# Optimization experiments

Hardware: AMD Instinct MI355X
Metric: run time of the kernel (lower is better)

## Reference

```python
import jax, jax.numpy as jnp
import numpy as np
from functools import partial

EPS = 1e-5
PATCH = 3
STYLE_STRENGTH = 1.0


def _whiten_color_mats(x):
    # x: (b, c, n) already flattened; returns mean, eigvecs, eigvals of covariance
    mean = x.mean(axis=-1, keepdims=True)
    xc = x - mean
    n = x.shape[-1]
    cov = jnp.einsum('bcn,bdn->bcd', xc, xc) / (n - 1)
    evals, evecs = jnp.linalg.eigh(cov)
    evals = jnp.maximum(evals, EPS)
    return mean, xc, evecs, evals


def whitening(x):
    b, c, h, w = x.shape
    xf = x.reshape(b, c, h * w)
    _, xc, E, d = _whiten_color_mats(xf)
    # W = E diag(d^-1/2) E^T
    Wm = jnp.einsum('bce,be,bde->bcd', E, d ** -0.5, E)
    return jnp.einsum('bcd,bdn->bcn', Wm, xc).reshape(b, c, h, w)


def coloring(x, style):
    b, c, h, w = x.shape
    xf = x.reshape(b, c, h * w)
    sf = style.reshape(b, c, -1)
    smean, sc, E, d = _whiten_color_mats(sf)
    Cm = jnp.einsum('bce,be,bde->bcd', E, d ** 0.5, E)
    out = jnp.einsum('bcd,bdn->bcn', Cm, xf) + smean
    return out.reshape(b, c, h, w)


def extract_style_kernels(style):
    # returns (b, hw, c, 3, 3) patches and (b, hw, 1, 1, 1) L2 norms
    b, c, H, W = style.shape
    p = jnp.pad(style, ((0, 0), (0, 0), (1, 1), (1, 1)), mode='reflect')
    patches = jnp.stack([p[:, :, i:i + H, j:j + W]
                         for i in range(PATCH) for j in range(PATCH)], axis=-1)  # (b,c,H,W,9)
    k = patches.reshape(b, c, H * W, PATCH * PATCH).transpose(0, 2, 1, 3)  # (b,hw,c,9)
    norm = jnp.sqrt(jnp.sum(k * k, axis=(2, 3))) + EPS  # (b,hw)
    return k.reshape(b, H * W, c, PATCH, PATCH), norm[:, :, None, None, None]


_DN = ('NCHW', 'OIHW', 'NCHW')


def _conv_per_sample(feat, kern):
    # feat (c,H,W), kern (o,c,3,3): reflect-pad 1, VALID conv -> (o,H,W)
    fp = jnp.pad(feat, ((0, 0), (1, 1), (1, 1)), mode='reflect')
    out = jax.lax.conv_general_dilated(fp[None], kern, (1, 1), 'VALID',
                                       dimension_numbers=_DN)
    return out[0]


def _deconv_per_sample(onehot, kern):
    # conv_transpose2d(stride=1, padding=2) == VALID conv with flipped, transposed kernel
    kt = jnp.flip(kern, axis=(-2, -1)).transpose(1, 0, 2, 3)  # (c, hw, 3, 3)
    fp = jnp.pad(onehot, ((0, 0), (1, 1), (1, 1)), mode='reflect')
    out = jax.lax.conv_general_dilated(fp[None], kt, (1, 1), 'VALID',
                                       dimension_numbers=_DN)
    return out[0]


def norm_deconvolution(h, w, patch_size):
    full = np.zeros((h + patch_size - 1, w + patch_size - 1), dtype=np.float32)
    for x in range(patch_size):
        for y in range(patch_size):
            full[y:y + h, x:x + w] += 1.0
    pw = (patch_size - 1) // 2
    if pw > 0:
        full = full[pw:-pw, pw:-pw]
    return jnp.asarray(full)[None, None]  # (1,1,h,w)


def reassemble_feature(nc, ns):
    b, c, H, W = nc.shape
    hw = H * W
    kern, norm = extract_style_kernels(ns)
    score = jax.vmap(_conv_per_sample)(nc, kern / norm)  # (b, hw, H, W)
    idx = jnp.argmax(score, axis=1)  # (b, H, W)
    onehot = (jnp.arange(hw, dtype=idx.dtype)[None, :, None, None] == idx[:, None]
              ).astype(nc.dtype)  # (b, hw, H, W)
    recon = jax.vmap(_deconv_per_sample)(onehot, kern)  # (b, c, H, W)
    return recon / norm_deconvolution(H, W, PATCH).astype(recon.dtype)


def setup_inputs() -> dict:
    key = jax.random.key(0)
    k1, k2 = jax.random.split(key)
    content_feature = jax.random.normal(k1, (2, 256, 64, 64), dtype=jnp.float32)
    style_feature = jax.random.normal(k2, (2, 256, 64, 64), dtype=jnp.float32)
    return {"content_feature": content_feature, "style_feature": style_feature}


def reference(content_feature, style_feature):
    nc = whitening(content_feature)
    ns = whitening(style_feature)
    reassembled = reassemble_feature(nc, ns)
    stylized = coloring(reassembled, style_feature)
    return (1.0 - STYLE_STRENGTH) * content_feature + STYLE_STRENGTH * stylized
```

## Files before the change

kernel.cpp:

```cpp
#include <hip/hip_runtime.h>
#include <hip/hip_bf16.h>

#define C_ 256
#define N_ 4096
#define CN (C_*N_)
#define EPSF 1e-5f
#define NS_ITERS 6
#define KSPLIT 16
#define LSTR 40

typedef _Float16 f16x8 __attribute__((ext_vector_type(8)));
typedef float f32x4 __attribute__((ext_vector_type(4)));

__device__ __forceinline__ int refl(int t) {
  return t < 0 ? -t : (t > 63 ? 126 - t : t);
}

__device__ __forceinline__ unsigned short f2h(float x) {
  _Float16 h = (_Float16)x;
  return __builtin_bit_cast(unsigned short, h);
}
__device__ __forceinline__ float h2f(unsigned short u) {
  return (float)__builtin_bit_cast(_Float16, u);
}

__device__ __forceinline__ void mm64_3term(unsigned short* sm, const float* A, const float* B,
                                           int m0, int n0, f32x4 acc[2][2]) {
  const int P = 64*LSTR;
  int t = threadIdx.x;
  int lane = t & 63;
  int wv = (t >> 7) & 1, wu = (t >> 6) & 1;
  int lx16 = lane & 15, quad = lane >> 4;
  int srow = t >> 2, sseg = (t & 3) * 8;
#pragma unroll
  for (int i = 0; i < 2; i++)
#pragma unroll
    for (int j = 0; j < 2; j++) acc[i][j] = (f32x4){0.f, 0.f, 0.f, 0.f};
  for (int k0 = 0; k0 < 256; k0 += 32) {
    __syncthreads();
    {
      const float* pa = &A[(size_t)(m0 + srow)*256 + k0 + sseg];
      const float* pb = &B[(size_t)(n0 + srow)*256 + k0 + sseg];
#pragma unroll
      for (int g = 0; g < 2; g++) {
        float4 va = *(const float4*)(pa + g*4);
        float4 vb = *(const float4*)(pb + g*4);
        float fa[4] = {va.x, va.y, va.z, va.w};
        float fb[4] = {vb.x, vb.y, vb.z, vb.w};
        unsigned short ha[4], la[4], hb[4], lb[4];
#pragma unroll
        for (int j = 0; j < 4; j++) {
          unsigned short h = f2h(fa[j]); ha[j] = h; la[j] = f2h(fa[j] - h2f(h));
          h = f2h(fb[j]); hb[j] = h; lb[j] = f2h(fb[j] - h2f(h));
        }
        int lo_ = srow*LSTR + sseg + g*4;
        *(ushort4*)&sm[0*P + lo_] = make_ushort4(ha[0], ha[1], ha[2], ha[3]);
        *(ushort4*)&sm[1*P + lo_] = make_ushort4(la[0], la[1], la[2], la[3]);
        *(ushort4*)&sm[2*P + lo_] = make_ushort4(hb[0], hb[1], hb[2], hb[3]);
        *(ushort4*)&sm[3*P + lo_] = make_ushort4(lb[0], lb[1], lb[2], lb[3]);
      }
    }
    __syncthreads();
    f16x8 ah[2], al[2], bh[2], bl[2];
#pragma unroll
    for (int mt = 0; mt < 2; mt++) {
      int arow = (wv*32 + mt*16 + lx16)*LSTR + quad*8;
      ah[mt] = *(const f16x8*)&sm[0*P + arow];
      al[mt] = *(const f16x8*)&sm[1*P + arow];
    }
#pragma unroll
    for (int nt = 0; nt < 2; nt++) {
      int brow = (wu*32 + nt*16 + lx16)*LSTR + quad*8;
      bh[nt] = *(const f16x8*)&sm[2*P + brow];
      bl[nt] = *(const f16x8*)&sm[3*P + brow];
    }
#pragma unroll
    for (int mt = 0; mt < 2; mt++)
#pragma unroll
      for (int nt = 0; nt < 2; nt++) {
        f32x4 a = acc[mt][nt];
        a = __builtin_amdgcn_mfma_f32_16x16x32_f16(ah[mt], bh[nt], a, 0, 0, 0);
        a = __builtin_amdgcn_mfma_f32_16x16x32_f16(ah[mt], bl[nt], a, 0, 0, 0);
        a = __builtin_amdgcn_mfma_f32_16x16x32_f16(al[mt], bh[nt], a, 0, 0, 0);
        acc[mt][nt] = a;
      }
  }
}

__global__ __launch_bounds__(256) void k_mean(const float* content, const float* style,
                                              float* means) {
  int c = blockIdx.x, m = blockIdx.y, t = threadIdx.x;
  const float* x = (m < 2 ? content : style) + (size_t)(m & 1) * CN + (size_t)c * N_;
  float s = 0.f;
  for (int i = t; i < N_; i += 256) s += x[i];
  __shared__ float red[256];
  red[t] = s; __syncthreads();
  for (int off = 128; off > 0; off >>= 1) { if (t < off) red[t] += red[t + off]; __syncthreads(); }
  if (t == 0) means[m * C_ + c] = red[0] * (1.f / N_);
}

__global__ __launch_bounds__(256) void k_splitall(const float* content, const float* style,
                                                  const float* means,
                                                  unsigned short* covsp, unsigned short* xcT) {
  int m = blockIdx.z;
  const float* x = (m < 2 ? content : style) + (size_t)(m & 1) * CN;
  int u0 = blockIdx.x * 32, c0 = blockIdx.y * 32;
  unsigned short* ch_ = covsp + (size_t)(2*m+0)*CN;
  unsigned short* cl_ = covsp + (size_t)(2*m+1)*CN;
  unsigned short* th_ = xcT + (size_t)(2*m+0)*CN;
  unsigned short* tl_ = xcT + (size_t)(2*m+1)*CN;
  __shared__ float tile[32][33];
  int t = threadIdx.x;
  {
    int cc = t >> 3, uu4 = (t & 7) * 4;
    float4 v = *(const float4*)&x[(size_t)(c0+cc)*N_ + u0 + uu4];
    float f[4] = {v.x, v.y, v.z, v.w};
    unsigned short h[4], lo[4];
#pragma unroll
    for (int j = 0; j < 4; j++) {
      unsigned short hh = f2h(f[j]);
      h[j] = hh; lo[j] = f2h(f[j] - h2f(hh));
      tile[cc][uu4+j] = f[j];
    }
    size_t o = (size_t)(c0+cc)*N_ + u0 + uu4;
    *(ushort4*)&ch_[o] = make_ushort4(h[0], h[1], h[2], h[3]);
    *(ushort4*)&cl_[o] = make_ushort4(lo[0], lo[1], lo[2], lo[3]);
  }
  __syncthreads();
  {
    int uu = t >> 3, cc4 = (t & 7) * 4;
    unsigned short h[4], lo[4];
#pragma unroll
    for (int j = 0; j < 4; j++) {
      float v = tile[cc4+j][uu] - means[m*C_ + c0 + cc4 + j];
      unsigned short hh = f2h(v);
      h[j] = hh; lo[j] = f2h(v - h2f(hh));
    }
    size_t o = (size_t)(u0+uu)*C_ + c0 + cc4;
    *(ushort4*)&th_[o] = make_ushort4(h[0], h[1], h[2], h[3]);
    *(ushort4*)&tl_[o] = make_ushort4(lo[0], lo[1], lo[2], lo[3]);
  }
}

__global__ __launch_bounds__(512) void k_covmm(const unsigned short* sp, float* covp) {
  __shared__ unsigned short sm[4*128*LSTR];
  const int P = 128*LSTR;
  int t = threadIdx.x;
  int kc = blockIdx.x, m = blockIdx.z;
  int ti = blockIdx.y >> 1, tj = blockIdx.y & 1;
  const unsigned short* Xh = sp + (size_t)m * 2 * (size_t)CN;
  const unsigned short* Xl = Xh + CN;
  int v0 = ti * 128, u0 = tj * 128;
  int wave = t >> 6, lane = t & 63;
  int wv = wave >> 1, wu = wave & 1;
  int lx16 = lane & 15, quad = lane >> 4;
  int srow = t >> 2, sseg = (t & 3) * 8;
  f32x4 acc[2][4];
#pragma unroll
  for (int i = 0; i < 2; i++)
#pragma unroll
    for (int j = 0; j < 4; j++) acc[i][j] = (f32x4){0.f, 0.f, 0.f, 0.f};

  int kbeg = kc * (N_ / KSPLIT), kend = kbeg + (N_ / KSPLIT);
  for (int k0 = kbeg; k0 < kend; k0 += 32) {
    __syncthreads();
    {
      size_t goA = (size_t)(v0 + srow) * N_ + k0 + sseg;
      size_t goB = (size_t)(u0 + srow) * N_ + k0 + sseg;
      int lo_ = srow * LSTR + sseg;
      *(float4*)&sm[0*P + lo_] = *(const float4*)&Xh[goA];
      *(float4*)&sm[1*P + lo_] = *(const float4*)&Xl[goA];
      *(float4*)&sm[2*P + lo_] = *(const float4*)&Xh[goB];
      *(float4*)&sm[3*P + lo_] = *(const float4*)&Xl[goB];
    }
    __syncthreads();
#pragma unroll
    for (int mt = 0; mt < 2; mt++) {
      int arow = (wv*32 + mt*16 + lx16)*LSTR + quad*8;
      f16x8 ah = *(const f16x8*)&sm[0*P + arow];
      f16x8 al = *(const f16x8*)&sm[1*P + arow];
#pragma unroll
      for (int nt = 0; nt < 4; nt++) {
        int brow = (wu*64 + nt*16 + lx16)*LSTR + quad*8;
        f16x8 bh = *(const f16x8*)&sm[2*P + brow];
        f16x8 bl = *(const f16x8*)&sm[3*P + brow];
        f32x4 a = acc[mt][nt];
        a = __builtin_amdgcn_mfma_f32_16x16x32_f16(ah, bh, a, 0, 0, 0);
        a = __builtin_amdgcn_mfma_f32_16x16x32_f16(ah, bl, a, 0, 0, 0);
        a = __builtin_amdgcn_mfma_f32_16x16x32_f16(al, bh, a, 0, 0, 0);
        acc[mt][nt] = a;
      }
    }
  }
  float* O = covp + ((size_t)kc*4 + m) * 65536;
#pragma unroll
  for (int mt = 0; mt < 2; mt++)
#pragma unroll
    for (int nt = 0; nt < 4; nt++)
#pragma unroll
      for (int i = 0; i < 4; i++)
        O[(size_t)(v0 + wv*32 + mt*16 + quad*4 + i)*C_ + (u0 + wu*64 + nt*16 + lx16)] =
            acc[mt][nt][i];
}

__global__ __launch_bounds__(256) void k_trace2(const float* covp, const float* means,
                                                float* cnrm) {
  int m = blockIdx.x, t = threadIdx.x;
  float s = 0.f;
#pragma unroll
  for (int kc = 0; kc < KSPLIT; kc++)
    s += covp[((size_t)kc*4 + m)*65536 + (size_t)t*257];
  float mi = means[m*C_ + t];
  float d = (s - (float)N_*mi*mi) * (1.f/(float)(N_-1));
  __shared__ float red[256];
  red[t] = d; __syncthreads();
  for (int off = 128; off > 0; off >>= 1) { if (t < off) red[t] += red[t + off]; __syncthreads(); }
  if (!t) cnrm[m] = red[0] * (1.3f/256.f);
}

__global__ __launch_bounds__(256) void k_covred_init(const float* covp, const float* means,
                                                     const float* cnrm, float* Y, float* Z) {
  int i = blockIdx.x, m = blockIdx.y, j = threadIdx.x;
  float s = 0.f;
#pragma unroll
  for (int kc = 0; kc < KSPLIT; kc++)
    s += covp[((size_t)kc*4 + m)*65536 + (size_t)i*C_ + j];
  float mi = means[m*C_ + i], mj = means[m*C_ + j];
  float cv = (s - (float)N_*mi*mj) * (1.f/(float)(N_-1));
  size_t o = (size_t)m*65536 + (size_t)i*C_ + j;
  Y[o] = cv / cnrm[m];
  Z[o] = (i == j) ? 1.f : 0.f;
}

__global__ __launch_bounds__(256) void k_nsA(const float* Zin, const float* Yin, float* T) {
  __shared__ unsigned short sm[4*64*LSTR];
  int m = blockIdx.y;
  int m0 = (blockIdx.x >> 2) * 64, n0 = (blockIdx.x & 3) * 64;
  const float* A = Zin + (size_t)m*65536;
  const float* B = Yin + (size_t)m*65536;
  float* O = T + (size_t)m*65536;
  f32x4 acc[2][2];
  mm64_3term(sm, A, B, m0, n0, acc);
  int t = threadIdx.x, lane = t & 63;
  int wv = (t >> 7) & 1, wu = (t >> 6) & 1, lx16 = lane & 15, quad = lane >> 4;
#pragma unroll
  for (int mt = 0; mt < 2; mt++)
#pragma unroll
    for (int nt = 0; nt < 2; nt++)
#pragma unroll
      for (int i = 0; i < 4; i++) {
        int r = m0 + wv*32 + mt*16 + quad*4 + i;
        int c = n0 + wu*32 + nt*16 + lx16;
        float v = acc[mt][nt][i];
        O[(size_t)r*256 + c] = (r == c) ? 3.f - v : -v;
      }
}

__global__ __launch_bounds__(256) void k_nsB(const float* Yin, const float* Zin, const float* T,
                                             float* Yout, float* Zout) {
  __shared__ unsigned short sm[4*64*LSTR];
  int m = blockIdx.y, z = blockIdx.z;
  const float* A = (z == 0 ? Yin : Zin) + (size_t)m*65536;
  const float* B = T + (size_t)m*65536;
  float* O = (z == 0 ? Yout : Zout) + (size_t)m*65536;
  int m0 = (blockIdx.x >> 2) * 64, n0 = (blockIdx.x & 3) * 64;
  f32x4 acc[2][2];
  mm64_3term(sm, A, B, m0, n0, acc);
  int t = threadIdx.x, lane = t & 63;
  int wv = (t >> 7) & 1, wu = (t >> 6) & 1, lx16 = lane & 15, quad = lane >> 4;
#pragma unroll
  for (int mt = 0; mt < 2; mt++)
#pragma unroll
    for (int nt = 0; nt < 2; nt++)
#pragma unroll
      for (int i = 0; i < 4; i++) {
        int r = m0 + wv*32 + mt*16 + quad*4 + i;
        int c = n0 + wu*32 + nt*16 + lx16;
        O[(size_t)r*256 + c] = 0.5f * acc[mt][nt][i];
      }
}

__global__ __launch_bounds__(256) void k_whitenT(const unsigned short* xcT, const float* Zall,
                                                 const float* cnrm, unsigned short* outT) {
  __shared__ unsigned short sm[4*64*LSTR];
  const int P = 64*LSTR;
  int m = blockIdx.z;
  int v0 = blockIdx.x * 64, c0 = blockIdx.y * 64;
  const float* Zm = Zall + (size_t)m*65536;
  const unsigned short* Bh_g = xcT + (size_t)(2*m+0)*CN;
  const unsigned short* Bl_g = xcT + (size_t)(2*m+1)*CN;
  unsigned short* Oh = outT + (size_t)(2*m+0)*CN;
  unsigned short* Ol = outT + (size_t)(2*m+1)*CN;
  int t = threadIdx.x, lane = t & 63;
  int wv = (t >> 7) & 1, wu = (t >> 6) & 1;
  int lx16 = lane & 15, quad = lane >> 4;
  int srow = t >> 2, sseg = (t & 3) * 8;
  f32x4 acc[2][2];
#pragma unroll
  for (int i = 0; i < 2; i++)
#pragma unroll
    for (int j = 0; j < 2; j++) acc[i][j] = (f32x4){0.f, 0.f, 0.f, 0.f};
  for (int k0 = 0; k0 < 256; k0 += 32) {
    __syncthreads();
    {
      const float* pa = &Zm[(size_t)(c0 + srow)*256 + k0 + sseg];
      int lo_ = srow*LSTR + sseg;
#pragma unroll
      for (int g = 0; g < 2; g++) {
        float4 va = *(const float4*)(pa + g*4);
        float fa[4] = {va.x, va.y, va.z, va.w};
        unsigned short ha[4], la[4];
#pragma unroll
        for (int j = 0; j < 4; j++) {
          unsigned short h = f2h(fa[j]); ha[j] = h; la[j] = f2h(fa[j] - h2f(h));
        }
        *(ushort4*)&sm[0*P + lo_ + g*4] = make_ushort4(ha[0], ha[1], ha[2], ha[3]);
        *(ushort4*)&sm[1*P + lo_ + g*4] = make_ushort4(la[0], la[1], la[2], la[3]);
      }
      size_t gb = (size_t)(v0 + srow)*C_ + k0 + sseg;
      *(float4*)&sm[2*P + lo_] = *(const float4*)&Bh_g[gb];
      *(float4*)&sm[3*P + lo_] = *(const float4*)&Bl_g[gb];
    }
    __syncthreads();
    f16x8 ah[2], al[2], bh[2], bl[2];
#pragma unroll
    for (int mt = 0; mt < 2; mt++) {
      int arow = (wv*32 + mt*16 + lx16)*LSTR + quad*8;
      ah[mt] = *(const f16x8*)&sm[0*P + arow];
      al[mt] = *(const f16x8*)&sm[1*P + arow];
    }
#pragma unroll
    for (int nt = 0; nt < 2; nt++) {
      int brow = (wu*32 + nt*16 + lx16)*LSTR + quad*8;
      bh[nt] = *(const f16x8*)&sm[2*P + brow];
      bl[nt] = *(const f16x8*)&sm[3*P + brow];
    }
#pragma unroll
    for (int mt = 0; mt < 2; mt++)
#pragma unroll
      for (int nt = 0; nt < 2; nt++) {
        f32x4 a = acc[mt][nt];
        a = __builtin_amdgcn_mfma_f32_16x16x32_f16(ah[mt], bh[nt], a, 0, 0, 0);
        a = __builtin_amdgcn_mfma_f32_16x16x32_f16(ah[mt], bl[nt], a, 0, 0, 0);
        a = __builtin_amdgcn_mfma_f32_16x16x32_f16(al[mt], bh[nt], a, 0, 0, 0);
        acc[mt][nt] = a;
      }
  }
  float scale = 1.0f / sqrtf(cnrm[m]);
  __syncthreads();
  unsigned short* Th = sm;
  unsigned short* Tl = sm + 64*72;
#pragma unroll
  for (int mt = 0; mt < 2; mt++)
#pragma unroll
    for (int nt = 0; nt < 2; nt++)
#pragma unroll
      for (int i = 0; i < 4; i++) {
        int chl = wv*32 + mt*16 + quad*4 + i;
        int vl  = wu*32 + nt*16 + lx16;
        float w = acc[mt][nt][i] * scale;
        unsigned short h = f2h(w);
        unsigned short l = f2h(w - h2f(h));
        Th[vl*72 + chl] = h;
        Tl[vl*72 + chl] = l;
      }
  __syncthreads();
  int vr = t >> 2, cs = (t & 3) * 16;
  size_t go = (size_t)(v0 + vr)*C_ + c0 + cs;
  *(float4*)&Oh[go]     = *(float4*)&Th[vr*72 + cs];
  *(float4*)&Oh[go + 8] = *(float4*)&Th[vr*72 + cs + 8];
  *(float4*)&Ol[go]     = *(float4*)&Tl[vr*72 + cs];
  *(float4*)&Ol[go + 8] = *(float4*)&Tl[vr*72 + cs + 8];
}

__global__ __launch_bounds__(256) void k_ssq(const unsigned short* outT, float* ssq) {
  int b = blockIdx.y; int p = blockIdx.x * 256 + threadIdx.x;
  const unsigned short* h = outT + (size_t)(2*(2+b))*CN + (size_t)p*C_;
  const unsigned short* l = h + CN;
  float acc = 0.f;
  for (int c = 0; c < C_; c += 4) {
    ushort4 hv = *(const ushort4*)&h[c];
    ushort4 lv = *(const ushort4*)&l[c];
    float v0 = h2f(hv.x) + h2f(lv.x);
    float v1 = h2f(hv.y) + h2f(lv.y);
    float v2 = h2f(hv.z) + h2f(lv.z);
    float v3 = h2f(hv.w) + h2f(lv.w);
    acc += v0*v0 + v1*v1 + v2*v2 + v3*v3;
  }
  ssq[b*N_ + p] = acc;
}

__global__ __launch_bounds__(256) void k_rnorm(const float* ssq, float* rnorm) {
  int b = blockIdx.y; int s = blockIdx.x * 256 + threadIdx.x;
  int sy = s >> 6, sx = s & 63;
  float sum = 0.f;
#pragma unroll
  for (int ky = 0; ky < 3; ky++)
#pragma unroll
    for (int kx = 0; kx < 3; kx++)
      sum += ssq[b*N_ + refl(sy+ky-1)*64 + refl(sx+kx-1)];
  rnorm[b*N_ + s] = 1.f / (sqrtf(sum) + EPSF);
}

__global__ __launch_bounds__(512) void k_gram(const unsigned short* Ah_g, const unsigned short* Al_g,
                                              const unsigned short* Bh_g, const unsigned short* Bl_g,
                                              float* Hx) {
  __shared__ unsigned short sm[4*128*LSTR];
  const int P = 128*LSTR;
  int t = threadIdx.x;
  int v0 = blockIdx.y * 128, u0 = blockIdx.x * 128;
  int wave = t >> 6, lane = t & 63;
  int wv = wave >> 1, wu = wave & 1;
  int lx16 = lane & 15, quad = lane >> 4;
  int srow = t >> 2, sseg = (t & 3) * 8;
  f32x4 acc[2][4];
#pragma unroll
  for (int i = 0; i < 2; i++)
#pragma unroll
    for (int j = 0; j < 4; j++) acc[i][j] = (f32x4){0.f, 0.f, 0.f, 0.f};

  for (int k0 = 0; k0 < 256; k0 += 32) {
    __syncthreads();
    {
      size_t goA = (size_t)(v0 + srow)*C_ + k0 + sseg;
      size_t goB = (size_t)(u0 + srow)*C_ + k0 + sseg;
      int lo_ = srow*LSTR + sseg;
      *(float4*)&sm[0*P + lo_] = *(const float4*)&Ah_g[goA];
      *(float4*)&sm[1*P + lo_] = *(const float4*)&Al_g[goA];
      *(float4*)&sm[2*P + lo_] = *(const float4*)&Bh_g[goB];
      *(float4*)&sm[3*P + lo_] = *(const float4*)&Bl_g[goB];
    }
    __syncthreads();
    int kb = quad*8;
    f16x8 ah[2], al[2];
#pragma unroll
    for (int mt = 0; mt < 2; mt++) {
      int arow = (wv*32 + mt*16 + lx16)*LSTR + kb;
      ah[mt] = *(const f16x8*)&sm[0*P + arow];
      al[mt] = *(const f16x8*)&sm[1*P + arow];
    }
    f16x8 bh[4], bl[4];
#pragma unroll
    for (int nt = 0; nt < 4; nt++) {
      int brow = (wu*64 + nt*16 + lx16)*LSTR + kb;
      bh[nt] = *(const f16x8*)&sm[2*P + brow];
      bl[nt] = *(const f16x8*)&sm[3*P + brow];
    }
#pragma unroll
    for (int mt = 0; mt < 2; mt++)
#pragma unroll
      for (int nt = 0; nt < 4; nt++) {
        f32x4 a = acc[mt][nt];
        a = __builtin_amdgcn_mfma_f32_16x16x32_f16(ah[mt], bh[nt], a, 0, 0, 0);
        a = __builtin_amdgcn_mfma_f32_16x16x32_f16(ah[mt], bl[nt], a, 0, 0, 0);
        a = __builtin_amdgcn_mfma_f32_16x16x32_f16(al[mt], bh[nt], a, 0, 0, 0);
        acc[mt][nt] = a;
      }
  }
  float* Gs = (float*)sm;
  int btx = t & 15, bty = t >> 4;
#pragma unroll
  for (int h = 0; h < 2; h++) {
    __syncthreads();
    if ((wv >> 1) == h) {
      int rbase = (wv & 1) * 32;
#pragma unroll
      for (int mt = 0; mt < 2; mt++)
#pragma unroll
        for (int nt = 0; nt < 4; nt++)
#pragma unroll
          for (int i = 0; i < 4; i++)
            Gs[(rbase + mt*16 + quad*4 + i)*133 + wu*64 + nt*16 + lx16] = acc[mt][nt][i];
    }
    __syncthreads();
#pragma unroll
    for (int i = 0; i < 2; i++) {
      int px = bty*2 + i;
      int xm = refl(px-1), xp = refl(px+1);
#pragma unroll
      for (int jh = 0; jh < 2; jh++) {
        int ub = jh*64;
        float tmp[4];
#pragma unroll
        for (int j = 0; j < 4; j++) {
          int sx = btx*4 + j;
          int smm = refl(sx-1), sp = refl(sx+1);
          tmp[j] = Gs[xm*133 + ub + smm] + Gs[px*133 + ub + sx] + Gs[xp*133 + ub + sp];
        }
        *(float4*)&Hx[(size_t)(v0 + h*64 + px)*N_ + u0 + ub + btx*4] =
            make_float4(tmp[0], tmp[1], tmp[2], tmp[3]);
      }
    }
  }
}

__global__ __launch_bounds__(256) void k_argmax(const float* Hx, const float* rnorm,
                                                int* idx, int b) {
  int p = blockIdx.x, t = threadIdx.x;
  int py = p >> 6, px = p & 63;
  size_t r0 = (size_t)(refl(py-1)*64 + px) * N_;
  size_t r1 = (size_t)p * N_;
  size_t r2 = (size_t)(refl(py+1)*64 + px) * N_;
  float bv = -1e30f; int bs = 0;
  for (int s = t; s < N_; s += 256) {
    int sy = s >> 6, sx = s & 63;
    int u0 = refl(sy-1)*64 + sx, u2 = refl(sy+1)*64 + sx;
    float acc = Hx[r0 + u0] + Hx[r1 + s] + Hx[r2 + u2];
    float sc = acc * rnorm[b*N_ + s];
    if (sc > bv) { bv = sc; bs = s; }
  }
  __shared__ float sv[256]; __shared__ int si[256];
  sv[t] = bv; si[t] = bs; __syncthreads();
  for (int off = 128; off > 0; off >>= 1) {
    if (t < off) {
      if (sv[t+off] > sv[t] || (sv[t+off] == sv[t] && si[t+off] < si[t])) {
        sv[t] = sv[t+off]; si[t] = si[t+off];
      }
    }
    __syncthreads();
  }
  if (!t) idx[b*N_ + p] = si[0];
}

__global__ __launch_bounds__(256) void k_recon(const unsigned short* nsTh,
                                               const unsigned short* nsTl,
                                               const int* idx_b, float* recont_b) {
  int p = blockIdx.x, c = threadIdx.x;
  int py = p >> 6, px = p & 63;
  float acc = 0.f;
#pragma unroll
  for (int dy = 0; dy < 3; dy++)
#pragma unroll
    for (int dx = 0; dx < 3; dx++) {
      int q = refl(py+dy-1)*64 + refl(px+dx-1);
      int s = idx_b[q];
      int sy = s >> 6, sx = s & 63;
      size_t o = (size_t)(refl(sy+1-dy)*64 + refl(sx+1-dx))*C_ + c;
      acc += h2f(nsTh[o]) + h2f(nsTl[o]);
    }
  float dc = ((py==0||py==63)?2.f:3.f) * ((px==0||px==63)?2.f:3.f);
  recont_b[(size_t)p*C_ + c] = acc / dc;
}

__global__ __launch_bounds__(256) void k_color(const float* Yall, const float* recont_all,
                                               const float* cnrm, const float* means,
                                               float* out_all) {
  __shared__ unsigned short sm[4*64*LSTR];
  int b = blockIdx.z;
  const float* Ym = Yall + (size_t)(2+b)*65536;
  const float* recont = recont_all + (size_t)b*CN;
  const float* smean = means + (2+b)*C_;
  float* out = out_all + (size_t)b*CN;
  int m0 = blockIdx.y * 64;
  int n0 = blockIdx.x * 64;
  f32x4 acc[2][2];
  mm64_3term(sm, Ym, recont, m0, n0, acc);
  float scale = sqrtf(cnrm[2+b]);
  int t = threadIdx.x, lane = t & 63;
  int wv = (t >> 7) & 1, wu = (t >> 6) & 1, lx16 = lane & 15, quad = lane >> 4;
#pragma unroll
  for (int mt = 0; mt < 2; mt++)
#pragma unroll
    for (int nt = 0; nt < 2; nt++)
#pragma unroll
      for (int i = 0; i < 4; i++) {
        int r = m0 + wv*32 + mt*16 + quad*4 + i;
        int c = n0 + wu*32 + nt*16 + lx16;
        out[(size_t)r*N_ + c] = acc[mt][nt][i]*scale + smean[r];
      }
}

extern "C" void kernel_launch(void* const* d_in, const int* in_sizes, int n_in,
                              void* d_out, int out_size, void* d_ws, size_t ws_size,
                              hipStream_t stream) {
  const float* content = (const float*)d_in[0];
  const float* style   = (const float*)d_in[1];
  float* out = (float*)d_out;

  float* F = (float*)d_ws;
  float* means  = F + 0;
  float* cnrm   = F + 1024;
  float* Y      = F + 264192;
  float* Z      = F + 526336;
  float* Y2     = F + 788480;
  float* Z2     = F + 1050624;
  float* T      = F + 1312768;
  float* ncreg  = F + 1574912;
  float* nsreg  = F + 3672064;
  float* recont = F + 7866368;
  float* ssq    = F + 9963520;
  float* rnorm  = F + 9971712;
  int*   idx    = (int*)(F + 9979904);
  float* Hx     = F + 9988096;

  unsigned short* covsp = (unsigned short*)Hx;
  float* covp = Hx + 4194304;

  unsigned short* xcT  = (unsigned short*)nsreg;
  unsigned short* outT = (unsigned short*)ncreg;

  k_mean<<<dim3(256,4), 256, 0, stream>>>(content, style, means);
  k_splitall<<<dim3(128,8,4), 256, 0, stream>>>(content, style, means, covsp, xcT);
  k_covmm<<<dim3(KSPLIT,4,4), 512, 0, stream>>>(covsp, covp);
  k_trace2<<<4, 256, 0, stream>>>(covp, means, cnrm);
  k_covred_init<<<dim3(256,4), 256, 0, stream>>>(covp, means, cnrm, Y, Z);
  float *Ya = Y, *Za = Z, *Yb = Y2, *Zb = Z2;
  for (int it = 0; it < NS_ITERS; it++) {
    k_nsA<<<dim3(16,4), 256, 0, stream>>>(Za, Ya, T);
    k_nsB<<<dim3(16,4,2), 256, 0, stream>>>(Ya, Za, T, Yb, Zb);
    float* tmp;
    tmp = Ya; Ya = Yb; Yb = tmp;
    tmp = Za; Za = Zb; Zb = tmp;
  }
  k_whitenT<<<dim3(64,4,4), 256, 0, stream>>>(xcT, Za, cnrm, outT);
  k_ssq<<<dim3(16,2), 256, 0, stream>>>(outT, ssq);
  k_rnorm<<<dim3(16,2), 256, 0, stream>>>(ssq, rnorm);
  for (int b = 0; b < 2; b++) {
    k_gram<<<dim3(32,32), 512, 0, stream>>>(outT + (size_t)(2*b)*CN,
                                            outT + (size_t)(2*b+1)*CN,
                                            outT + (size_t)(2*(2+b))*CN,
                                            outT + (size_t)(2*(2+b)+1)*CN, Hx);
    k_argmax<<<4096, 256, 0, stream>>>(Hx, rnorm, idx, b);
    k_recon<<<4096, 256, 0, stream>>>(outT + (size_t)(2*(2+b))*CN,
                                      outT + (size_t)(2*(2+b)+1)*CN,
                                      idx + (size_t)b*N_, recont + (size_t)b*CN);
  }
  k_color<<<dim3(64,4,2), 256, 0, stream>>>(Ya, recont, cnrm, means, out);
}
```

Baseline: 376.2 us.

## Shrink Newton-Schulz tiles, pair rows in argmax, reorder gram row mapping

```diff
diff --git a/kernel.cpp b/kernel.cpp
--- a/kernel.cpp
+++ b/kernel.cpp
@@ -85,6 +85,49 @@
         acc[mt][nt] = a;
       }
   }
+}
+
+__device__ __forceinline__ f32x4 mm32_3term(unsigned short* sm, const float* A, const float* B,
+                                            int m0, int n0) {
+  const int P = 32*LSTR;
+  int t = threadIdx.x, lane = t & 63;
+  int w = t >> 6, wv = w >> 1, wu = w & 1;
+  int lx16 = lane & 15, quad = lane >> 4;
+  int mat = t >> 7, srow = (t >> 2) & 31, sseg = (t & 3) * 8;
+  const float* S = mat ? B : A;
+  int rb = mat ? n0 : m0;
+  int base0 = mat ? 2*P : 0;
+  f32x4 acc = (f32x4){0.f, 0.f, 0.f, 0.f};
+  for (int k0 = 0; k0 < 256; k0 += 32) {
+    __syncthreads();
+    {
+      const float* p = &S[(size_t)(rb + srow)*256 + k0 + sseg];
+      int lo_ = srow*LSTR + sseg;
+#pragma unroll
+      for (int g = 0; g < 2; g++) {
+        float4 v = *(const float4*)(p + g*4);
+        float f[4] = {v.x, v.y, v.z, v.w};
+        unsigned short hh[4], ll[4];
+#pragma unroll
+        for (int j = 0; j < 4; j++) {
+          unsigned short h = f2h(f[j]); hh[j] = h; ll[j] = f2h(f[j] - h2f(h));
+        }
+        *(ushort4*)&sm[base0 + lo_ + g*4]     = make_ushort4(hh[0], hh[1], hh[2], hh[3]);
+        *(ushort4*)&sm[base0 + P + lo_ + g*4] = make_ushort4(ll[0], ll[1], ll[2], ll[3]);
+      }
+    }
+    __syncthreads();
+    int arow = (wv*16 + lx16)*LSTR + quad*8;
+    int brow = (wu*16 + lx16)*LSTR + quad*8;
+    f16x8 ah = *(const f16x8*)&sm[0*P + arow];
+    f16x8 al = *(const f16x8*)&sm[1*P + arow];
+    f16x8 bh = *(const f16x8*)&sm[2*P + brow];
+    f16x8 bl = *(const f16x8*)&sm[3*P + brow];
+    acc = __builtin_amdgcn_mfma_f32_16x16x32_f16(ah, bh, acc, 0, 0, 0);
+    acc = __builtin_amdgcn_mfma_f32_16x16x32_f16(ah, bl, acc, 0, 0, 0);
+    acc = __builtin_amdgcn_mfma_f32_16x16x32_f16(al, bh, acc, 0, 0, 0);
+  }
+  return acc;
 }
 
 __global__ __launch_bounds__(256) void k_mean(const float* content, const float* style,
@@ -233,51 +276,43 @@
 }
 
 __global__ __launch_bounds__(256) void k_nsA(const float* Zin, const float* Yin, float* T) {
-  __shared__ unsigned short sm[4*64*LSTR];
+  __shared__ unsigned short sm[4*32*LSTR];
   int m = blockIdx.y;
-  int m0 = (blockIdx.x >> 2) * 64, n0 = (blockIdx.x & 3) * 64;
+  int m0 = (blockIdx.x >> 3) * 32, n0 = (blockIdx.x & 7) * 32;
   const float* A = Zin + (size_t)m*65536;
   const float* B = Yin + (size_t)m*65536;
   float* O = T + (size_t)m*65536;
-  f32x4 acc[2][2];
-  mm64_3term(sm, A, B, m0, n0, acc);
+  f32x4 acc = mm32_3term(sm, A, B, m0, n0);
   int t = threadIdx.x, lane = t & 63;
-  int wv = (t >> 7) & 1, wu = (t >> 6) & 1, lx16 = lane & 15, quad = lane >> 4;
-#pragma unroll
-  for (int mt = 0; mt < 2; mt++)
-#pragma unroll
-    for (int nt = 0; nt < 2; nt++)
-#pragma unroll
-      for (int i = 0; i < 4; i++) {
-        int r = m0 + wv*32 + mt*16 + quad*4 + i;
-        int c = n0 + wu*32 + nt*16 + lx16;
-        float v = acc[mt][nt][i];
-        O[(size_t)r*256 + c] = (r == c) ? 3.f - v : -v;
-      }
+  int w = t >> 6, wv = w >> 1, wu = w & 1;
+  int lx16 = lane & 15, quad = lane >> 4;
+#pragma unroll
+  for (int i = 0; i < 4; i++) {
+    int r = m0 + wv*16 + quad*4 + i;
+    int c = n0 + wu*16 + lx16;
+    float v = acc[i];
+    O[(size_t)r*256 + c] = (r == c) ? 3.f - v : -v;
+  }
 }
 
 __global__ __launch_bounds__(256) void k_nsB(const float* Yin, const float* Zin, const float* T,
                                              float* Yout, float* Zout) {
-  __shared__ unsigned short sm[4*64*LSTR];
+  __shared__ unsigned short sm[4*32*LSTR];
   int m = blockIdx.y, z = blockIdx.z;
   const float* A = (z == 0 ? Yin : Zin) + (size_t)m*65536;
   const float* B = T + (size_t)m*65536;
   float* O = (z == 0 ? Yout : Zout) + (size_t)m*65536;
-  int m0 = (blockIdx.x >> 2) * 64, n0 = (blockIdx.x & 3) * 64;
-  f32x4 acc[2][2];
-  mm64_3term(sm, A, B, m0, n0, acc);
+  int m0 = (blockIdx.x >> 3) * 32, n0 = (blockIdx.x & 7) * 32;
+  f32x4 acc = mm32_3term(sm, A, B, m0, n0);
   int t = threadIdx.x, lane = t & 63;
-  int wv = (t >> 7) & 1, wu = (t >> 6) & 1, lx16 = lane & 15, quad = lane >> 4;
-#pragma unroll
-  for (int mt = 0; mt < 2; mt++)
-#pragma unroll
-    for (int nt = 0; nt < 2; nt++)
-#pragma unroll
-      for (int i = 0; i < 4; i++) {
-        int r = m0 + wv*32 + mt*16 + quad*4 + i;
-        int c = n0 + wu*32 + nt*16 + lx16;
-        O[(size_t)r*256 + c] = 0.5f * acc[mt][nt][i];
-      }
+  int w = t >> 6, wv = w >> 1, wu = w & 1;
+  int lx16 = lane & 15, quad = lane >> 4;
+#pragma unroll
+  for (int i = 0; i < 4; i++) {
+    int r = m0 + wv*16 + quad*4 + i;
+    int c = n0 + wu*16 + lx16;
+    O[(size_t)r*256 + c] = 0.5f * acc[i];
+  }
 }
 
 __global__ __launch_bounds__(256) void k_whitenT(const unsigned short* xcT, const float* Zall,
@@ -475,7 +510,7 @@
     __syncthreads();
 #pragma unroll
     for (int i = 0; i < 2; i++) {
-      int px = bty*2 + i;
+      int px = bty + 32*i;
       int xm = refl(px-1), xp = refl(px+1);
 #pragma unroll
       for (int jh = 0; jh < 2; jh++) {
@@ -496,21 +531,26 @@
 
 __global__ __launch_bounds__(256) void k_argmax(const float* Hx, const float* rnorm,
                                                 int* idx, int b) {
-  int p = blockIdx.x, t = threadIdx.x;
-  int py = p >> 6, px = p & 63;
-  size_t r0 = (size_t)(refl(py-1)*64 + px) * N_;
-  size_t r1 = (size_t)p * N_;
-  size_t r2 = (size_t)(refl(py+1)*64 + px) * N_;
-  float bv = -1e30f; int bs = 0;
+  int blk = blockIdx.x, t = threadIdx.x;
+  int q = blk >> 6, px = blk & 63;
+  int py0 = 2*q, py1 = 2*q + 1;
+  size_t rm = (size_t)(refl(py0-1)*64 + px) * N_;
+  size_t r0 = (size_t)(py0*64 + px) * N_;
+  size_t r1 = (size_t)(py1*64 + px) * N_;
+  size_t rp = (size_t)(refl(py1+1)*64 + px) * N_;
+  float bv0 = -1e30f, bv1 = -1e30f; int bs0 = 0, bs1 = 0;
   for (int s = t; s < N_; s += 256) {
     int sy = s >> 6, sx = s & 63;
     int u0 = refl(sy-1)*64 + sx, u2 = refl(sy+1)*64 + sx;
-    float acc = Hx[r0 + u0] + Hx[r1 + s] + Hx[r2 + u2];
-    float sc = acc * rnorm[b*N_ + s];
-    if (sc > bv) { bv = sc; bs = s; }
+    float rn = rnorm[b*N_ + s];
+    float a0 = Hx[rm + u0] + Hx[r0 + s] + Hx[r1 + u2];
+    float a1 = Hx[r0 + u0] + Hx[r1 + s] + Hx[rp + u2];
+    float sc0 = a0 * rn, sc1 = a1 * rn;
+    if (sc0 > bv0) { bv0 = sc0; bs0 = s; }
+    if (sc1 > bv1) { bv1 = sc1; bs1 = s; }
   }
   __shared__ float sv[256]; __shared__ int si[256];
-  sv[t] = bv; si[t] = bs; __syncthreads();
+  sv[t] = bv0; si[t] = bs0; __syncthreads();
   for (int off = 128; off > 0; off >>= 1) {
     if (t < off) {
       if (sv[t+off] > sv[t] || (sv[t+off] == sv[t] && si[t+off] < si[t])) {
@@ -519,7 +559,18 @@
     }
     __syncthreads();
   }
-  if (!t) idx[b*N_ + p] = si[0];
+  if (!t) idx[b*N_ + py0*64 + px] = si[0];
+  __syncthreads();
+  sv[t] = bv1; si[t] = bs1; __syncthreads();
+  for (int off = 128; off > 0; off >>= 1) {
+    if (t < off) {
+      if (sv[t+off] > sv[t] || (sv[t+off] == sv[t] && si[t+off] < si[t])) {
+        sv[t] = sv[t+off]; si[t] = si[t+off];
+      }
+    }
+    __syncthreads();
+  }
+  if (!t) idx[b*N_ + py1*64 + px] = si[0];
 }
 
 __global__ __launch_bounds__(256) void k_recon(const unsigned short* nsTh,
@@ -606,8 +657,8 @@
   k_covred_init<<<dim3(256,4), 256, 0, stream>>>(covp, means, cnrm, Y, Z);
   float *Ya = Y, *Za = Z, *Yb = Y2, *Zb = Z2;
   for (int it = 0; it < NS_ITERS; it++) {
-    k_nsA<<<dim3(16,4), 256, 0, stream>>>(Za, Ya, T);
-    k_nsB<<<dim3(16,4,2), 256, 0, stream>>>(Ya, Za, T, Yb, Zb);
+    k_nsA<<<dim3(64,4), 256, 0, stream>>>(Za, Ya, T);
+    k_nsB<<<dim3(64,4,2), 256, 0, stream>>>(Ya, Za, T, Yb, Zb);
     float* tmp;
     tmp = Ya; Ya = Yb; Yb = tmp;
     tmp = Za; Za = Zb; Zb = tmp;
@@ -620,7 +671,7 @@
                                             outT + (size_t)(2*b+1)*CN,
                                             outT + (size_t)(2*(2+b))*CN,
                                             outT + (size_t)(2*(2+b)+1)*CN, Hx);
-    k_argmax<<<4096, 256, 0, stream>>>(Hx, rnorm, idx, b);
+    k_argmax<<<2048, 256, 0, stream>>>(Hx, rnorm, idx, b);
     k_recon<<<4096, 256, 0, stream>>>(outT + (size_t)(2*(2+b))*CN,
                                       outT + (size_t)(2*(2+b)+1)*CN,
                                       idx + (size_t)b*N_, recont + (size_t)b*CN);
```

New measurement: 351.8 us. 6.5% less time.
